# Kernel optimization log

Hardware: AMD Instinct MI355X
Metric: run time of the kernel (lower is better)

The kernel has to match this reference:

```python
import jax, jax.numpy as jnp
import numpy as np

EPS = 1e-5
K = 20
H = [64, 64, 128, 256]

def knn_idx(x, k):
    # x: [B,N,3] -> idx [B,N,k] of nearest neighbors by squared euclidean distance
    inner = -2.0 * jnp.einsum('bnc,bmc->bnm', x, x)
    x2 = jnp.sum(x * x, axis=-1)                      # [B,N]
    neg_d = -x2[:, :, None] - inner - x2[:, None, :]  # -||xi-xj||^2
    _, idx = jax.lax.top_k(neg_d, k)
    return idx

def edge_features(x, idx):
    # x: [B,N,C], idx: [B,N,k] -> [B,N,k,2C] = concat(neighbor - center, center)
    nbr = jax.vmap(lambda xb, ib: xb[ib])(x, idx)     # [B,N,k,C]
    ctr = jnp.broadcast_to(x[:, :, None, :], nbr.shape)
    return jnp.concatenate([nbr - ctr, ctr], axis=-1)

def edge_conv(e, W, b, g, be):
    # e: [B,N,k,Cin]; 1x1 Conv2d == einsum; BatchNorm2d (batch stats) + LeakyReLU(0.2)
    h = jnp.einsum('bnkc,oc->bnko', e, W) + b
    m = jnp.mean(h, axis=(0, 1, 2))
    v = jnp.var(h, axis=(0, 1, 2))
    h = g * (h - m) / jnp.sqrt(v + EPS) + be
    h = jnp.where(h >= 0, h, 0.2 * h)
    return jnp.max(h, axis=2)                          # max over k -> [B,N,O]

def setup_inputs() -> dict:
    key = jax.random.key(0)
    ks = jax.random.split(key, 32)
    B, N = 8, 2048
    d = {"x": jax.random.normal(ks[0], (B, N, 3), dtype=jnp.float32)}
    ins = [2 * 3, 2 * H[0], 2 * H[1], 2 * H[2]]
    for i in range(4):
        o, c = H[i], ins[i]
        d[f"W{i}"] = jax.random.normal(ks[1 + 4 * i], (o, c), dtype=jnp.float32) / np.sqrt(c)
        d[f"b{i}"] = jnp.zeros((o,), dtype=jnp.float32)
        d[f"g{i}"] = jnp.ones((o,), dtype=jnp.float32)
        d[f"be{i}"] = jnp.zeros((o,), dtype=jnp.float32)
    cin, cout = sum(H), 2 * 512
    d["Wf"] = jax.random.normal(ks[20], (cout, cin), dtype=jnp.float32) / np.sqrt(cin)
    d["bf"] = jnp.zeros((cout,), dtype=jnp.float32)
    return d

def reference(x, W0, b0, g0, be0, W1, b1, g1, be1, W2, b2, g2, be2, W3, b3, g3, be3, Wf, bf):
    params = [(W0, b0, g0, be0), (W1, b1, g1, be1), (W2, b2, g2, be2), (W3, b3, g3, be3)]
    xs = []
    h = x  # [B,N,C]
    for (W, b, g, be) in params:
        idx = knn_idx(h if h.shape[-1] != 3 else h, K) if h.shape[-1] == 3 else knn_idx(h, K)
        e = edge_features(h, idx)
        h = edge_conv(e, W, b, g, be)
        xs.append(h)
    xcat = jnp.concatenate(xs, axis=-1)               # [B,N,512]
    out = jnp.einsum('bnc,oc->bno', xcat, Wf) + bf    # 1x1 Conv1d
    return jnp.max(out, axis=1)                        # global max pool -> [B,1024]
```

## Files before the change

### kernel.cpp

```cpp
#include <hip/hip_runtime.h>
#include <cstdint>
#include <cstddef>


constexpr int NB = 8;
constexpr int NP = 2048;
constexpr int KK = 20;

typedef short bf16x8 __attribute__((ext_vector_type(8)));
typedef float f32x16 __attribute__((ext_vector_type(16)));

__device__ __forceinline__ f32x16 MF(bf16x8 a, bf16x8 b, f32x16 c) {
  return __builtin_amdgcn_mfma_f32_32x32x16_bf16(a, b, c, 0, 0, 0);
}
__device__ __forceinline__ unsigned short bfh(float f) {
  return (unsigned short)(__float_as_uint(f) >> 16);
}
__device__ __forceinline__ float bff(unsigned short u) {
  return __uint_as_float(((unsigned)u) << 16);
}
__device__ __forceinline__ void split2(float v, unsigned short& h, unsigned short& l) {
  h = bfh(v); l = bfh(v - bff(h));
}

#define FMA16(AV, BV, ACC)                                          \
  {                                                                 \
    const float _a[4] = {AV.x, AV.y, AV.z, AV.w};                   \
    const float _b[4] = {BV.x, BV.y, BV.z, BV.w};                   \
    _Pragma("unroll")                                               \
    for (int _e = 0; _e < 4; ++_e) {                                \
      _Pragma("unroll")                                             \
      for (int _f = 0; _f < 4; ++_f)                                \
        ACC[_e][_f] = fmaf(_a[_e], _b[_f], ACC[_e][_f]);            \
    }                                                               \
  }

__global__ __launch_bounds__(256) void pad_norms(const float* __restrict__ x,
    float* __restrict__ x4, float* __restrict__ nrm) {
  const int p = blockIdx.x * 256 + threadIdx.x;
  float4 v;
  v.x = x[p * 3 + 0]; v.y = x[p * 3 + 1]; v.z = x[p * 3 + 2]; v.w = 0.f;
  *reinterpret_cast<float4*>(x4 + (size_t)p * 4) = v;
  nrm[p] = v.x * v.x + v.y * v.y + v.z * v.z;
}

__global__ __launch_bounds__(256) void wsplit_all(const float* __restrict__ W1,
    const float* __restrict__ W2, const float* __restrict__ W3,
    const float* __restrict__ Wf,
    unsigned short* __restrict__ wb1, unsigned short* __restrict__ wb2,
    unsigned short* __restrict__ wb3,
    unsigned short* __restrict__ wfh, unsigned short* __restrict__ wfl) {
  const int id = blockIdx.x * 256 + threadIdx.x;
  if (id < 524288) {
    const int row = id >> 9, c = id & 511;
    unsigned short h, l;
    split2(Wf[id], h, l);
    const size_t a = ((((size_t)(row >> 6)) * 64 + (c >> 3)) * 64 + (row & 63)) * 8 + (c & 7);
    wfh[a] = h; wfl[a] = l;
    return;
  }
  int id2 = id - 524288;
  const float* W; unsigned short* wb; int O, C;
  if (id2 < 4096)      { W = W1; wb = wb1; O = 64;  C = 64;  }
  else if (id2 < 12288){ W = W2; wb = wb2; O = 128; C = 64;  id2 -= 4096; }
  else                 { W = W3; wb = wb3; O = 256; C = 128; id2 -= 12288; }
  const int o = id2 / C, c = id2 % C;
  const int K8 = C >> 3;
  const float w1 = W[o * 2 * C + c];
  const float w2 = W[o * 2 * C + C + c];
  unsigned short h, l;
  const int r1 = o, rd = O + o;
  const size_t a1 = (((size_t)(r1 >> 6) * K8 + (c >> 3)) * 64 + (r1 & 63)) * 8 + (c & 7);
  const size_t ad = (((size_t)(rd >> 6) * K8 + (c >> 3)) * 64 + (rd & 63)) * 8 + (c & 7);
  split2(w1, h, l);
  wb[a1] = h; wb[2 * O * C + a1] = l;
  split2(w2 - w1, h, l);
  wb[ad] = h; wb[2 * O * C + ad] = l;
}

__global__ __launch_bounds__(256) void dist0_kernel(const float* __restrict__ X4,
    const float* __restrict__ norms, float* __restrict__ negd, int bbase) {
  __shared__ float sb[640];
  const int t = threadIdx.x, tr = t & 15, tcq = t >> 4;
  const int z = blockIdx.z, b = bbase + z;
  const int i0 = blockIdx.x * 64, j0 = blockIdx.y * 64;
  const int c4 = t >> 6, row = t & 63;
  if (t < 64) sb[512 + t] = norms[b * NP + i0 + t];
  else if (t < 128) sb[512 + t] = norms[b * NP + j0 + (t - 64)];
  sb[c4 * 64 + row] = X4[(size_t)(b * NP + i0 + row) * 4 + c4];
  sb[256 + c4 * 64 + row] = X4[(size_t)(b * NP + j0 + row) * 4 + c4];
  __syncthreads();
  float acc[4][4] = {};
#pragma unroll
  for (int c = 0; c < 4; ++c) {
    const float4 a = *reinterpret_cast<const float4*>(sb + c * 64 + tr * 4);
    const float4 bb = *reinterpret_cast<const float4*>(sb + 256 + c * 64 + tcq * 4);
    FMA16(a, bb, acc);
  }
#pragma unroll
  for (int e = 0; e < 4; ++e) {
    const int rowi = tr * 4 + e;
    const float ni = sb[512 + rowi];
    float4 nd;
    nd.x = 2.f * acc[e][0] - ni - sb[576 + tcq * 4 + 0];
    nd.y = 2.f * acc[e][1] - ni - sb[576 + tcq * 4 + 1];
    nd.z = 2.f * acc[e][2] - ni - sb[576 + tcq * 4 + 2];
    nd.w = 2.f * acc[e][3] - ni - sb[576 + tcq * 4 + 3];
    *reinterpret_cast<float4*>(negd + ((size_t)z * NP + i0 + rowi) * NP + j0 + tcq * 4) = nd;
  }
}

template<int C>
__global__ __launch_bounds__(256) void dist_mfma(const unsigned short* __restrict__ xh,
    const unsigned short* __restrict__ xl, int colbase,
    const float* __restrict__ norms, float* __restrict__ negd, int bbase) {
  constexpr int H = C / 16;
  const int t = threadIdx.x, lane = t & 63, w = t >> 6;
  const int half = lane >> 5, l31 = lane & 31;
  const int rt = (w >> 1) * 32, tc = (w & 1) * 32;
  const int z = blockIdx.z, b = bbase + z;
  const int i0 = blockIdx.x * 64, j0 = blockIdx.y * 64;
  const int ti = (b * NP + i0) >> 6, tj = (b * NP + j0) >> 6;
  const int k8b = colbase >> 3;
  const int col = tc + l31;

  bf16x8 BH[H], BL[H];
#pragma unroll
  for (int ch = 0; ch < H; ++ch) {
    const size_t a = (((size_t)tj * 64 + k8b + ch * 2 + half) * 64 + col) * 8;
    BH[ch] = *reinterpret_cast<const bf16x8*>(xh + a);
    BL[ch] = *reinterpret_cast<const bf16x8*>(xl + a);
  }

  f32x16 acc;
#pragma unroll
  for (int i = 0; i < 16; ++i) acc[i] = 0.f;
#pragma unroll
  for (int ch = 0; ch < H; ++ch) {
    const size_t a = (((size_t)ti * 64 + k8b + ch * 2 + half) * 64 + rt + l31) * 8;
    const bf16x8 ah = *reinterpret_cast<const bf16x8*>(xh + a);
    const bf16x8 al = *reinterpret_cast<const bf16x8*>(xl + a);
    acc = MF(ah, BH[ch], acc); acc = MF(ah, BL[ch], acc); acc = MF(al, BH[ch], acc);
  }

  const float nj = norms[b * NP + j0 + col];
#pragma unroll
  for (int i = 0; i < 16; ++i) {
    const int row = rt + (i & 3) + 8 * (i >> 2) + 4 * half;
    const float ni = norms[b * NP + i0 + row];
    negd[((size_t)z * NP + i0 + row) * NP + j0 + col] = 2.f * acc[i] - ni - nj;
  }
}

__global__ __launch_bounds__(256) void knn_select_kernel(const float* __restrict__ negd,
    int* __restrict__ idxout, int bbase) {
  const int t = threadIdx.x, lane = t & 63, w = t >> 6;
  const int rloc = blockIdx.x * 4 + w;
  const float* rowp = negd + (size_t)rloc * NP + lane * 32;

  float v[32];
#pragma unroll
  for (int m = 0; m < 8; ++m) {
    const float4 d = *reinterpret_cast<const float4*>(rowp + m * 4);
    v[m * 4 + 0] = d.x; v[m * 4 + 1] = d.y; v[m * 4 + 2] = d.z; v[m * 4 + 3] = d.w;
  }
  float lm = v[0]; int lp = 0;
#pragma unroll
  for (int e = 1; e < 32; ++e)
    if (v[e] > lm) { lm = v[e]; lp = e; }

  int* op = idxout + (size_t)(bbase * NP + rloc) * KK;
  for (int r = 0; r < KK; ++r) {
    float wm = lm;
#pragma unroll
    for (int o = 1; o < 64; o <<= 1) wm = fmaxf(wm, __shfl_xor(wm, o));
    const unsigned long long bal = __ballot(lm == wm);
    const int wl = __ffsll(bal) - 1;
    if (lane == wl) {
      op[r] = lane * 32 + lp;
#pragma unroll
      for (int e = 0; e < 32; ++e)
        if (e == lp) v[e] = -__builtin_inff();
      lm = v[0]; lp = 0;
#pragma unroll
      for (int e = 1; e < 32; ++e)
        if (v[e] > lm) { lm = v[e]; lp = e; }
    }
  }
}

__global__ __launch_bounds__(256) void pt_gemm0(const float* __restrict__ x,
    const float* __restrict__ W, const float* __restrict__ bias,
    float* __restrict__ Y, float* __restrict__ T) {
  const int t = threadIdx.x;
  const int o = t & 63;
  const int g = blockIdx.x * 4 + (t >> 6);
  const float x0 = x[(size_t)g * 3 + 0], x1 = x[(size_t)g * 3 + 1], x2 = x[(size_t)g * 3 + 2];
  const float w10 = W[o * 6 + 0], w11 = W[o * 6 + 1], w12 = W[o * 6 + 2];
  const float w20 = W[o * 6 + 3], w21 = W[o * 6 + 4], w22 = W[o * 6 + 5];
  Y[(size_t)g * 64 + o] = w10 * x0 + w11 * x1 + w12 * x2;
  T[(size_t)g * 64 + o] = (w20 - w10) * x0 + (w21 - w11) * x1 + (w22 - w12) * x2 + bias[o];
}

template<int C, int O2>
__global__ __launch_bounds__(256) void pt_gemm(const unsigned short* __restrict__ xh,
    const unsigned short* __restrict__ xl, int colbase,
    const unsigned short* __restrict__ wch, const unsigned short* __restrict__ wcl,
    const float* __restrict__ bias, float* __restrict__ Y, float* __restrict__ T) {
  constexpr int K8 = C / 8;
  constexpr int H = K8 / 2;
  constexpr int O = O2 / 2;
  const int t = threadIdx.x, lane = t & 63, w = t >> 6;
  const int half = lane >> 5, l31 = lane & 31;
  const int rt = (w >> 1) * 32, tc = (w & 1) * 32;
  const int n0 = blockIdx.x * 64, o0 = blockIdx.y * 64;
  const int tn = n0 >> 6, to = o0 >> 6;
  const int k8b = colbase >> 3;
  const int col = o0 + tc + l31;

  bf16x8 BH[H], BL[H];
#pragma unroll
  for (int ch = 0; ch < H; ++ch) {
    const size_t a = (((size_t)to * K8 + ch * 2 + half) * 64 + tc + l31) * 8;
    BH[ch] = *reinterpret_cast<const bf16x8*>(wch + a);
    BL[ch] = *reinterpret_cast<const bf16x8*>(wcl + a);
  }

  f32x16 acc;
#pragma unroll
  for (int i = 0; i < 16; ++i) acc[i] = 0.f;
#pragma unroll
  for (int ch = 0; ch < H; ++ch) {
    const size_t a = (((size_t)tn * 64 + k8b + ch * 2 + half) * 64 + rt + l31) * 8;
    const bf16x8 ah = *reinterpret_cast<const bf16x8*>(xh + a);
    const bf16x8 al = *reinterpret_cast<const bf16x8*>(xl + a);
    acc = MF(ah, BH[ch], acc); acc = MF(ah, BL[ch], acc); acc = MF(al, BH[ch], acc);
  }

  if (col < O) {
#pragma unroll
    for (int i = 0; i < 16; ++i) {
      const int row = n0 + rt + (i & 3) + 8 * (i >> 2) + 4 * half;
      Y[(size_t)row * O + col] = acc[i];
    }
  } else {
    const float bv = bias[col - O];
#pragma unroll
    for (int i = 0; i < 16; ++i) {
      const int row = n0 + rt + (i & 3) + 8 * (i >> 2) + 4 * half;
      T[(size_t)row * O + (col - O)] = acc[i] + bv;
    }
  }
}

template<int O>
__global__ __launch_bounds__(256) void edge_reduce(const float* __restrict__ Y,
    const float* __restrict__ T, const int* __restrict__ idx,
    float* __restrict__ outmax, float* __restrict__ ssum, float* __restrict__ ssq) {
  constexpr int PTS = 32;
  constexpr int NG = 256 / O;
  const int t = threadIdx.x;
  const int o = t % O, ng = t / O;
  const int g0 = blockIdx.x * PTS;
  float sacc = 0.f, qacc = 0.f;
  for (int p = ng; p < PTS; p += NG) {
    const int g = g0 + p;
    const int b = g >> 11;
    const float tv = T[(size_t)g * O + o];
    const int* ip = idx + (size_t)g * KK;
    int ji[KK];
#pragma unroll
    for (int k = 0; k < KK; ++k) ji[k] = ip[k];
    float vs[KK];
#pragma unroll
    for (int k = 0; k < KK; ++k) vs[k] = Y[(size_t)(b * NP + ji[k]) * O + o];
    float mx = -__builtin_inff();
#pragma unroll
    for (int k = 0; k < KK; ++k) {
      const float h = vs[k] + tv;
      mx = fmaxf(mx, h);
      sacc += h;
      qacc = fmaf(h, h, qacc);
    }
    outmax[(size_t)g * O + o] = mx;
  }
  atomicAdd(ssum + o, sacc);
  atomicAdd(ssq + o, qacc);
}

template<int O, bool WN>
__global__ __launch_bounds__(256) void bnrelu_kernel(const float* __restrict__ fA,
    const float* __restrict__ ssum, const float* __restrict__ ssq,
    const float* __restrict__ g, const float* __restrict__ be,
    unsigned short* __restrict__ xh, unsigned short* __restrict__ xl, int colbase,
    float* __restrict__ nrm) {
  constexpr float INV = 1.0f / 327680.0f;
  constexpr int K8 = O / 8;
  const int id = blockIdx.x * 256 + threadIdx.x;
  const int r = id & 63;
  const int k8loc = (id >> 6) % K8;
  const int tile = (id >> 6) / K8;
  const int n = tile * 64 + r;
  const int c0 = k8loc * 8;

  float hv[8];
  {
    const float4 p0 = *reinterpret_cast<const float4*>(fA + (size_t)n * O + c0);
    const float4 p1 = *reinterpret_cast<const float4*>(fA + (size_t)n * O + c0 + 4);
    hv[0] = p0.x; hv[1] = p0.y; hv[2] = p0.z; hv[3] = p0.w;
    hv[4] = p1.x; hv[5] = p1.y; hv[6] = p1.z; hv[7] = p1.w;
  }
  unsigned short hh[8], ll[8];
  float s = 0.f;
#pragma unroll
  for (int j = 0; j < 8; ++j) {
    const int col = c0 + j;
    const float m = ssum[col] * INV;
    const float v = ssq[col] * INV - m * m;
    const float sc = g[col] / sqrtf(v + 1e-5f);
    float val = (hv[j] - m) * sc + be[col];
    val = (val >= 0.f) ? val : 0.2f * val;
    split2(val, hh[j], ll[j]);
    const float recon = bff(hh[j]) + bff(ll[j]);
    s = fmaf(recon, recon, s);
  }
  const size_t ob = (((size_t)tile * 64 + (colbase >> 3) + k8loc) * 64 + r) * 8;
  uint4 ph, pl;
  ph.x = (unsigned)hh[0] | ((unsigned)hh[1] << 16);
  ph.y = (unsigned)hh[2] | ((unsigned)hh[3] << 16);
  ph.z = (unsigned)hh[4] | ((unsigned)hh[5] << 16);
  ph.w = (unsigned)hh[6] | ((unsigned)hh[7] << 16);
  pl.x = (unsigned)ll[0] | ((unsigned)ll[1] << 16);
  pl.y = (unsigned)ll[2] | ((unsigned)ll[3] << 16);
  pl.z = (unsigned)ll[4] | ((unsigned)ll[5] << 16);
  pl.w = (unsigned)ll[6] | ((unsigned)ll[7] << 16);
  *reinterpret_cast<uint4*>(xh + ob) = ph;
  *reinterpret_cast<uint4*>(xl + ob) = pl;
  if (WN) atomicAdd(nrm + n, s);
}

__global__ __launch_bounds__(256) void final_mfma(const unsigned short* __restrict__ xh,
    const unsigned short* __restrict__ xl, const unsigned short* __restrict__ wfh,
    const unsigned short* __restrict__ wfl, unsigned* __restrict__ outenc) {
  __shared__ float fr[128];
  const int t = threadIdx.x, lane = t & 63, w = t >> 6;
  const int half = lane >> 5, l31 = lane & 31;
  const int rt = (w >> 1) * 32, tc = (w & 1) * 32;
  const int b = blockIdx.z, n0 = blockIdx.x * 64, o0 = blockIdx.y * 64;
  const int tn = (b * NP + n0) >> 6, to = o0 >> 6;

  f32x16 acc;
#pragma unroll
  for (int i = 0; i < 16; ++i) acc[i] = 0.f;

  for (int cc = 0; cc < 4; ++cc) {
    bf16x8 BH[8], BL[8];
#pragma unroll
    for (int ch = 0; ch < 8; ++ch) {
      const int k8 = cc * 16 + ch * 2 + half;
      const size_t a = (((size_t)to * 64 + k8) * 64 + tc + l31) * 8;
      BH[ch] = *reinterpret_cast<const bf16x8*>(wfh + a);
      BL[ch] = *reinterpret_cast<const bf16x8*>(wfl + a);
    }
#pragma unroll
    for (int ch = 0; ch < 8; ++ch) {
      const int k8 = cc * 16 + ch * 2 + half;
      const size_t a = (((size_t)tn * 64 + k8) * 64 + rt + l31) * 8;
      const bf16x8 ah = *reinterpret_cast<const bf16x8*>(xh + a);
      const bf16x8 al = *reinterpret_cast<const bf16x8*>(xl + a);
      acc = MF(ah, BH[ch], acc); acc = MF(ah, BL[ch], acc); acc = MF(al, BH[ch], acc);
    }
  }

  float M = acc[0];
#pragma unroll
  for (int i = 1; i < 16; ++i) M = fmaxf(M, acc[i]);
  M = fmaxf(M, __shfl_xor(M, 32));
  fr[w * 32 + l31] = M;
  __syncthreads();
  if (t < 64) {
    const float Mc = fmaxf(fr[t], fr[64 + t]);
    const unsigned ub = __float_as_uint(Mc);
    const unsigned key = (ub & 0x80000000u) ? ~ub : (ub | 0x80000000u);
    atomicMax(outenc + b * 1024 + o0 + t, key);
  }
}

__global__ __launch_bounds__(256) void decode_kernel(const unsigned int* __restrict__ enc,
    const float* __restrict__ bf, float* __restrict__ out) {
  const int gid = blockIdx.x * 256 + threadIdx.x;
  const unsigned key = enc[gid];
  const unsigned ubits = (key & 0x80000000u) ? (key & 0x7fffffffu) : ~key;
  out[gid] = __uint_as_float(ubits) + bf[gid & 1023];
}

extern "C" void kernel_launch(void* const* d_in, const int* in_sizes, int n_in,
                              void* d_out, int out_size, void* d_ws, size_t ws_size,
                              hipStream_t stream) {
  (void)in_sizes; (void)n_in; (void)out_size; (void)ws_size;
  const float* x   = (const float*)d_in[0];
  const float* W0  = (const float*)d_in[1];
  const float* b0  = (const float*)d_in[2];
  const float* g0  = (const float*)d_in[3];
  const float* be0 = (const float*)d_in[4];
  const float* W1  = (const float*)d_in[5];
  const float* b1  = (const float*)d_in[6];
  const float* g1  = (const float*)d_in[7];
  const float* be1 = (const float*)d_in[8];
  const float* W2  = (const float*)d_in[9];
  const float* b2  = (const float*)d_in[10];
  const float* g2  = (const float*)d_in[11];
  const float* be2 = (const float*)d_in[12];
  const float* W3  = (const float*)d_in[13];
  const float* b3  = (const float*)d_in[14];
  const float* g3  = (const float*)d_in[15];
  const float* be3 = (const float*)d_in[16];
  const float* Wf  = (const float*)d_in[17];
  const float* bf  = (const float*)d_in[18];

  float* wsf = (float*)d_ws;
  int* idxb = (int*)d_ws;
  float* stats = wsf + 327680;
  float* nb = wsf + 329728;
  unsigned* outenc = (unsigned*)(wsf + 395264);
  float* x4 = wsf + 403456;
  float* featA = wsf + 468992;
  float* negd = wsf + 4663296;
  float* Yb = negd;
  float* Tb = negd + 4194304;
  unsigned short* xh = (unsigned short*)(wsf + 21440512);
  unsigned short* xl = xh + 8388608;
  unsigned short* wb1 = xl + 8388608;
  unsigned short* wb2 = wb1 + 16384;
  unsigned short* wb3 = wb2 + 32768;
  unsigned short* wfh = wb3 + 131072;
  unsigned short* wfl = wfh + 524288;

  float* normsA = nb, *normsB = nb + 16384, *normsC = nb + 32768, *normsD = nb + 49152;

  hipMemsetAsync(stats, 0, (2048 + 65536) * sizeof(float), stream);
  hipMemsetAsync(outenc, 0, 8192 * sizeof(unsigned), stream);

  const dim3 blk(256, 1, 1);
  const dim3 ggrid(32, 32, 4);
  const dim3 sgrid(2048, 1, 1);
  const dim3 ergrid(512, 1, 1);

  pad_norms<<<dim3(64), blk, 0, stream>>>(x, x4, normsA);
  wsplit_all<<<dim3(2224), blk, 0, stream>>>(W1, W2, W3, Wf, wb1, wb2, wb3, wfh, wfl);

  for (int cb = 0; cb < 2; ++cb) {
    dist0_kernel<<<ggrid, blk, 0, stream>>>(x4, normsA, negd, 4 * cb);
    knn_select_kernel<<<sgrid, blk, 0, stream>>>(negd, idxb, 4 * cb);
  }
  pt_gemm0<<<dim3(4096), blk, 0, stream>>>(x, W0, b0, Yb, Tb);
  edge_reduce<64><<<ergrid, blk, 0, stream>>>(Yb, Tb, idxb, featA, stats, stats + 256);
  bnrelu_kernel<64, true><<<dim3(512), blk, 0, stream>>>(featA, stats, stats + 256,
      g0, be0, xh, xl, 0, normsB);

  for (int cb = 0; cb < 2; ++cb) {
    dist_mfma<64><<<ggrid, blk, 0, stream>>>(xh, xl, 0, normsB, negd, 4 * cb);
    knn_select_kernel<<<sgrid, blk, 0, stream>>>(negd, idxb, 4 * cb);
  }
  pt_gemm<64, 128><<<dim3(256, 2), blk, 0, stream>>>(xh, xl, 0, wb1, wb1 + 8192, b1, Yb, Tb);
  edge_reduce<64><<<ergrid, blk, 0, stream>>>(Yb, Tb, idxb, featA, stats + 512, stats + 768);
  bnrelu_kernel<64, true><<<dim3(512), blk, 0, stream>>>(featA, stats + 512, stats + 768,
      g1, be1, xh, xl, 64, normsC);

  for (int cb = 0; cb < 2; ++cb) {
    dist_mfma<64><<<ggrid, blk, 0, stream>>>(xh, xl, 64, normsC, negd, 4 * cb);
    knn_select_kernel<<<sgrid, blk, 0, stream>>>(negd, idxb, 4 * cb);
  }
  pt_gemm<64, 256><<<dim3(256, 4), blk, 0, stream>>>(xh, xl, 64, wb2, wb2 + 16384, b2, Yb, Tb);
  edge_reduce<128><<<ergrid, blk, 0, stream>>>(Yb, Tb, idxb, featA, stats + 1024, stats + 1280);
  bnrelu_kernel<128, true><<<dim3(1024), blk, 0, stream>>>(featA, stats + 1024, stats + 1280,
      g2, be2, xh, xl, 128, normsD);

  for (int cb = 0; cb < 2; ++cb) {
    dist_mfma<128><<<ggrid, blk, 0, stream>>>(xh, xl, 128, normsD, negd, 4 * cb);
    knn_select_kernel<<<sgrid, blk, 0, stream>>>(negd, idxb, 4 * cb);
  }
  pt_gemm<128, 512><<<dim3(256, 8), blk, 0, stream>>>(xh, xl, 128, wb3, wb3 + 65536, b3, Yb, Tb);
  edge_reduce<256><<<ergrid, blk, 0, stream>>>(Yb, Tb, idxb, featA, stats + 1536, stats + 1792);
  bnrelu_kernel<256, false><<<dim3(2048), blk, 0, stream>>>(featA, stats + 1536, stats + 1792,
      g3, be3, xh, xl, 256, nullptr);

  final_mfma<<<dim3(32, 16, 8), blk, 0, stream>>>(xh, xl, wfh, wfl, outenc);
  decode_kernel<<<dim3(32), blk, 0, stream>>>(outenc, bf, (float*)d_out);
}
```

Baseline: 1.027 ms.

## Reuse A tiles across column tiles in distance, LDS-stage knn rows, widen final GEMM tile

The distance MFMA kernel now loops over several 64-column tiles per block. For C=64 it keeps the row operand in registers and reloads only the column operand, which cuts repeated global loads and the number of blocks. The knn selector now loads each row with coalesced float4 reads into padded shared memory before each lane gathers its 32 contiguous values, replacing the strided per-lane global reads. The final GEMM processes two 64-point row tiles per block so each weight fragment is reused twice. In exchange there is more register pressure, fewer blocks in flight, and 33 KB of LDS per select block.

```diff
diff --git a/kernel.cpp b/kernel.cpp
--- a/kernel.cpp
+++ b/kernel.cpp
@@ -110,7 +110,7 @@
   }
 }
 
-template<int C>
+template<int C, int JT, bool HOLD>
 __global__ __launch_bounds__(256) void dist_mfma(const unsigned short* __restrict__ xh,
     const unsigned short* __restrict__ xl, int colbase,
     const float* __restrict__ norms, float* __restrict__ negd, int bbase) {
@@ -119,51 +119,84 @@
   const int half = lane >> 5, l31 = lane & 31;
   const int rt = (w >> 1) * 32, tc = (w & 1) * 32;
   const int z = blockIdx.z, b = bbase + z;
-  const int i0 = blockIdx.x * 64, j0 = blockIdx.y * 64;
-  const int ti = (b * NP + i0) >> 6, tj = (b * NP + j0) >> 6;
+  const int i0 = blockIdx.x * 64;
+  const int ti = (b * NP + i0) >> 6;
   const int k8b = colbase >> 3;
   const int col = tc + l31;
 
-  bf16x8 BH[H], BL[H];
-#pragma unroll
-  for (int ch = 0; ch < H; ++ch) {
-    const size_t a = (((size_t)tj * 64 + k8b + ch * 2 + half) * 64 + col) * 8;
-    BH[ch] = *reinterpret_cast<const bf16x8*>(xh + a);
-    BL[ch] = *reinterpret_cast<const bf16x8*>(xl + a);
-  }
-
-  f32x16 acc;
-#pragma unroll
-  for (int i = 0; i < 16; ++i) acc[i] = 0.f;
-#pragma unroll
-  for (int ch = 0; ch < H; ++ch) {
-    const size_t a = (((size_t)ti * 64 + k8b + ch * 2 + half) * 64 + rt + l31) * 8;
-    const bf16x8 ah = *reinterpret_cast<const bf16x8*>(xh + a);
-    const bf16x8 al = *reinterpret_cast<const bf16x8*>(xl + a);
-    acc = MF(ah, BH[ch], acc); acc = MF(ah, BL[ch], acc); acc = MF(al, BH[ch], acc);
-  }
-
-  const float nj = norms[b * NP + j0 + col];
+  bf16x8 AH[HOLD ? H : 1], AL[HOLD ? H : 1];
+  if constexpr (HOLD) {
+#pragma unroll
+    for (int ch = 0; ch < H; ++ch) {
+      const size_t a = (((size_t)ti * 64 + k8b + ch * 2 + half) * 64 + rt + l31) * 8;
+      AH[ch] = *reinterpret_cast<const bf16x8*>(xh + a);
+      AL[ch] = *reinterpret_cast<const bf16x8*>(xl + a);
+    }
+  }
+  float ni[16];
 #pragma unroll
   for (int i = 0; i < 16; ++i) {
     const int row = rt + (i & 3) + 8 * (i >> 2) + 4 * half;
-    const float ni = norms[b * NP + i0 + row];
-    negd[((size_t)z * NP + i0 + row) * NP + j0 + col] = 2.f * acc[i] - ni - nj;
+    ni[i] = norms[b * NP + i0 + row];
+  }
+
+  for (int jt = 0; jt < JT; ++jt) {
+    const int j0 = (blockIdx.y * JT + jt) * 64;
+    const int tj = (b * NP + j0) >> 6;
+    bf16x8 BH[H], BL[H];
+#pragma unroll
+    for (int ch = 0; ch < H; ++ch) {
+      const size_t a = (((size_t)tj * 64 + k8b + ch * 2 + half) * 64 + col) * 8;
+      BH[ch] = *reinterpret_cast<const bf16x8*>(xh + a);
+      BL[ch] = *reinterpret_cast<const bf16x8*>(xl + a);
+    }
+    const float nj = norms[b * NP + j0 + col];
+
+    f32x16 acc;
+#pragma unroll
+    for (int i = 0; i < 16; ++i) acc[i] = 0.f;
+#pragma unroll
+    for (int ch = 0; ch < H; ++ch) {
+      bf16x8 ah, al;
+      if constexpr (HOLD) {
+        ah = AH[ch]; al = AL[ch];
+      } else {
+        const size_t a = (((size_t)ti * 64 + k8b + ch * 2 + half) * 64 + rt + l31) * 8;
+        ah = *reinterpret_cast<const bf16x8*>(xh + a);
+        al = *reinterpret_cast<const bf16x8*>(xl + a);
+      }
+      acc = MF(ah, BH[ch], acc); acc = MF(ah, BL[ch], acc); acc = MF(al, BH[ch], acc);
+    }
+#pragma unroll
+    for (int i = 0; i < 16; ++i) {
+      const int row = rt + (i & 3) + 8 * (i >> 2) + 4 * half;
+      negd[((size_t)z * NP + i0 + row) * NP + j0 + col] = 2.f * acc[i] - ni[i] - nj;
+    }
   }
 }
 
 __global__ __launch_bounds__(256) void knn_select_kernel(const float* __restrict__ negd,
     int* __restrict__ idxout, int bbase) {
+  __shared__ float sb[4 * 2112];
   const int t = threadIdx.x, lane = t & 63, w = t >> 6;
   const int rloc = blockIdx.x * 4 + w;
-  const float* rowp = negd + (size_t)rloc * NP + lane * 32;
-
+  const float* rowp = negd + (size_t)rloc * NP;
+  float* ws = sb + w * 2112;
+
+#pragma unroll
+  for (int m = 0; m < 8; ++m) {
+    const int c = m * 256 + lane * 4;
+    const float4 d = *reinterpret_cast<const float4*>(rowp + c);
+    const int lo = c >> 5, e = c & 31;
+    ws[lo * 33 + e + 0] = d.x;
+    ws[lo * 33 + e + 1] = d.y;
+    ws[lo * 33 + e + 2] = d.z;
+    ws[lo * 33 + e + 3] = d.w;
+  }
   float v[32];
 #pragma unroll
-  for (int m = 0; m < 8; ++m) {
-    const float4 d = *reinterpret_cast<const float4*>(rowp + m * 4);
-    v[m * 4 + 0] = d.x; v[m * 4 + 1] = d.y; v[m * 4 + 2] = d.z; v[m * 4 + 3] = d.w;
-  }
+  for (int e = 0; e < 32; ++e) v[e] = ws[lane * 33 + e];
+
   float lm = v[0]; int lp = 0;
 #pragma unroll
   for (int e = 1; e < 32; ++e)
@@ -346,12 +379,12 @@
   const int t = threadIdx.x, lane = t & 63, w = t >> 6;
   const int half = lane >> 5, l31 = lane & 31;
   const int rt = (w >> 1) * 32, tc = (w & 1) * 32;
-  const int b = blockIdx.z, n0 = blockIdx.x * 64, o0 = blockIdx.y * 64;
+  const int b = blockIdx.z, n0 = blockIdx.x * 128, o0 = blockIdx.y * 64;
   const int tn = (b * NP + n0) >> 6, to = o0 >> 6;
 
-  f32x16 acc;
-#pragma unroll
-  for (int i = 0; i < 16; ++i) acc[i] = 0.f;
+  f32x16 acc0, acc1;
+#pragma unroll
+  for (int i = 0; i < 16; ++i) { acc0[i] = 0.f; acc1[i] = 0.f; }
 
   for (int cc = 0; cc < 4; ++cc) {
     bf16x8 BH[8], BL[8];
@@ -368,13 +401,21 @@
       const size_t a = (((size_t)tn * 64 + k8) * 64 + rt + l31) * 8;
       const bf16x8 ah = *reinterpret_cast<const bf16x8*>(xh + a);
       const bf16x8 al = *reinterpret_cast<const bf16x8*>(xl + a);
-      acc = MF(ah, BH[ch], acc); acc = MF(ah, BL[ch], acc); acc = MF(al, BH[ch], acc);
-    }
-  }
-
-  float M = acc[0];
-#pragma unroll
-  for (int i = 1; i < 16; ++i) M = fmaxf(M, acc[i]);
+      acc0 = MF(ah, BH[ch], acc0); acc0 = MF(ah, BL[ch], acc0); acc0 = MF(al, BH[ch], acc0);
+    }
+#pragma unroll
+    for (int ch = 0; ch < 8; ++ch) {
+      const int k8 = cc * 16 + ch * 2 + half;
+      const size_t a = (((size_t)(tn + 1) * 64 + k8) * 64 + rt + l31) * 8;
+      const bf16x8 ah = *reinterpret_cast<const bf16x8*>(xh + a);
+      const bf16x8 al = *reinterpret_cast<const bf16x8*>(xl + a);
+      acc1 = MF(ah, BH[ch], acc1); acc1 = MF(ah, BL[ch], acc1); acc1 = MF(al, BH[ch], acc1);
+    }
+  }
+
+  float M = fmaxf(acc0[0], acc1[0]);
+#pragma unroll
+  for (int i = 1; i < 16; ++i) M = fmaxf(M, fmaxf(acc0[i], acc1[i]));
   M = fmaxf(M, __shfl_xor(M, 32));
   fr[w * 32 + l31] = M;
   __syncthreads();
@@ -442,7 +483,6 @@
   hipMemsetAsync(outenc, 0, 8192 * sizeof(unsigned), stream);
 
   const dim3 blk(256, 1, 1);
-  const dim3 ggrid(32, 32, 4);
   const dim3 sgrid(2048, 1, 1);
   const dim3 ergrid(512, 1, 1);
 
@@ -450,7 +490,7 @@
   wsplit_all<<<dim3(2224), blk, 0, stream>>>(W1, W2, W3, Wf, wb1, wb2, wb3, wfh, wfl);
 
   for (int cb = 0; cb < 2; ++cb) {
-    dist0_kernel<<<ggrid, blk, 0, stream>>>(x4, normsA, negd, 4 * cb);
+    dist0_kernel<<<dim3(32, 32, 4), blk, 0, stream>>>(x4, normsA, negd, 4 * cb);
     knn_select_kernel<<<sgrid, blk, 0, stream>>>(negd, idxb, 4 * cb);
   }
   pt_gemm0<<<dim3(4096), blk, 0, stream>>>(x, W0, b0, Yb, Tb);
@@ -459,7 +499,7 @@
       g0, be0, xh, xl, 0, normsB);
 
   for (int cb = 0; cb < 2; ++cb) {
-    dist_mfma<64><<<ggrid, blk, 0, stream>>>(xh, xl, 0, normsB, negd, 4 * cb);
+    dist_mfma<64, 4, true><<<dim3(32, 8, 4), blk, 0, stream>>>(xh, xl, 0, normsB, negd, 4 * cb);
     knn_select_kernel<<<sgrid, blk, 0, stream>>>(negd, idxb, 4 * cb);
   }
   pt_gemm<64, 128><<<dim3(256, 2), blk, 0, stream>>>(xh, xl, 0, wb1, wb1 + 8192, b1, Yb, Tb);
@@ -468,7 +508,7 @@
       g1, be1, xh, xl, 64, normsC);
 
   for (int cb = 0; cb < 2; ++cb) {
-    dist_mfma<64><<<ggrid, blk, 0, stream>>>(xh, xl, 64, normsC, negd, 4 * cb);
+    dist_mfma<64, 4, true><<<dim3(32, 8, 4), blk, 0, stream>>>(xh, xl, 64, normsC, negd, 4 * cb);
     knn_select_kernel<<<sgrid, blk, 0, stream>>>(negd, idxb, 4 * cb);
   }
   pt_gemm<64, 256><<<dim3(256, 4), blk, 0, stream>>>(xh, xl, 64, wb2, wb2 + 16384, b2, Yb, Tb);
@@ -477,7 +517,7 @@
       g2, be2, xh, xl, 128, normsD);
 
   for (int cb = 0; cb < 2; ++cb) {
-    dist_mfma<128><<<ggrid, blk, 0, stream>>>(xh, xl, 128, normsD, negd, 4 * cb);
+    dist_mfma<128, 2, false><<<dim3(32, 16, 4), blk, 0, stream>>>(xh, xl, 128, normsD, negd, 4 * cb);
     knn_select_kernel<<<sgrid, blk, 0, stream>>>(negd, idxb, 4 * cb);
   }
   pt_gemm<128, 512><<<dim3(256, 8), blk, 0, stream>>>(xh, xl, 128, wb3, wb3 + 65536, b3, Yb, Tb);
@@ -485,6 +525,6 @@
   bnrelu_kernel<256, false><<<dim3(2048), blk, 0, stream>>>(featA, stats + 1536, stats + 1792,
       g3, be3, xh, xl, 256, nullptr);
 
-  final_mfma<<<dim3(32, 16, 8), blk, 0, stream>>>(xh, xl, wfh, wfl, outenc);
+  final_mfma<<<dim3(16, 16, 8), blk, 0, stream>>>(xh, xl, wfh, wfl, outenc);
   decode_kernel<<<dim3(32), blk, 0, stream>>>(outenc, bf, (float*)d_out);
 }
```

New measurement: 1.033 ms. No clear change (+0.6%).
